# Performance work log

Hardware: AMD Instinct MI355X
Metric: run time of the kernel (lower is better)

## Reference

```python
import jax, jax.numpy as jnp
import numpy as np

B, T, D, HD = 8, 2048, 1024, 64

def setup_inputs() -> dict:
    key = jax.random.key(0)
    k1, k2, k3, k4 = jax.random.split(key, 4)
    x = jax.random.normal(k1, (B, T, D), dtype=jnp.float32)
    Wq = jax.random.normal(k2, (D, HD), dtype=jnp.float32) * (D ** -0.5)
    Wk = jax.random.normal(k3, (D, HD), dtype=jnp.float32) * (D ** -0.5)
    Wv = jax.random.normal(k4, (D, HD), dtype=jnp.float32) * (D ** -0.5)
    return {"x": x, "Wq": Wq, "Wk": Wk, "Wv": Wv}

def reference(x, Wq, Wk, Wv):
    # x: [B,T,D]; projections: [D,HD]
    q = jnp.einsum('btd,dh->bth', x, Wq)
    k = jnp.einsum('btd,dh->bth', x, Wk)
    v = jnp.einsum('btd,dh->bth', x, Wv)
    hd = q.shape[-1]
    scores = jnp.einsum('bth,bsh->bts', q, k) * (hd ** -0.5)  # [B,T,T]
    t = scores.shape[-1]
    causal = jnp.tril(jnp.ones((t, t), dtype=bool))
    scores = jnp.where(causal, scores, -jnp.inf)
    w = jax.nn.softmax(scores, axis=-1)
    # dropout p=0.0 (eval) -> identity
    return jnp.einsum('bts,bsh->bth', w, v)
```

## Files before the change

kernel.cpp:

```cpp
#include <hip/hip_runtime.h>
#include <hip/hip_bf16.h>
#include <stdint.h>

#define NB 8
#define TT 2048
#define DD 1024
#define HDIM 64

typedef __bf16 bf16x8 __attribute__((ext_vector_type(8)));
typedef float f32x4 __attribute__((ext_vector_type(4)));

static_assert(sizeof(bf16x8) == 16, "bf16x8 must be 16 bytes");

__device__ inline ushort f2bf_bits(float f) {
    __hip_bfloat16 h = __float2bfloat16(f);
    return *reinterpret_cast<ushort*>(&h);
}
__device__ inline float bfbits2f(ushort u) {
    unsigned v = ((unsigned)u) << 16;
    return __builtin_bit_cast(float, v);
}
__device__ inline bf16x8 ldb8(const ushort* p) {
    return *reinterpret_cast<const bf16x8*>(p);
}

typedef __attribute__((address_space(3))) uint32_t lds_u32;
typedef const __attribute__((address_space(1))) uint32_t glb_u32;
__device__ inline void gl_lds16(const void* g, void* l) {
    __builtin_amdgcn_global_load_lds((glb_u32*)g, (lds_u32*)l, 16, 0, 0);
}

#define WCNT_VM2   0xF72
#define WCNT_VM3   0xF73
#define WCNT_VM4   0xF74
#define WCNT_LGKM0 0xC07F

__device__ inline int probe_f32(const ushort* x) {
    int lane = threadIdx.x & 63;
    int wild = 0;
    #pragma unroll
    for (int j = 0; j < 4; ++j) {
        ushort u = x[(lane * 4 + j) * 32];
        int e = (u >> 7) & 0xFF;
        wild += (e >= 0xC0);
    }
    unsigned long long m = __ballot(wild > 0);
    return __popcll(m) > 8;
}

__global__ __launch_bounds__(256) void k_wt(const ushort* __restrict__ x,
                                            const void* __restrict__ Wq,
                                            const void* __restrict__ Wk,
                                            const void* __restrict__ Wv,
                                            ushort* __restrict__ Wt) {
    int f32m = probe_f32(x);
    int idx = blockIdx.x * 256 + threadIdx.x;
    int mat = idx >> 16;
    int rem = idx & 65535;
    int d = rem >> 6;
    int h = rem & 63;
    const void* W = (mat == 0) ? Wq : (mat == 1) ? Wk : Wv;
    float v;
    if (f32m) v = ((const float*)W)[rem];
    else      v = bfbits2f(((const ushort*)W)[rem]);
    if (mat == 0) v *= 0.18033688011112042f;
    Wt[(size_t)mat * 65536 + (size_t)h * DD + d] = f2bf_bits(v);
}

template <int F32M>
__device__ inline void proj_body(const void* __restrict__ xv,
                                 const ushort* __restrict__ Wt,
                                 ushort* __restrict__ Qw,
                                 ushort* __restrict__ Kw,
                                 ushort* __restrict__ Vtw,
                                 ushort* Bf, float* Af) {
    int tid  = threadIdx.x;
    int w    = tid >> 6;
    int lane = tid & 63;
    int quad = lane >> 4;
    int col  = lane & 15;
    int mt   = w >> 2;
    int nh   = w & 3;
    int m0   = blockIdx.x * 32;

    ushort* Afb = (ushort*)Af;

    auto stage = [&](int buf, int kkk) {
        #pragma unroll
        for (int j = 0; j < 3; ++j) {
            int f  = w * 3 + j;
            int nt = f >> 1, ks = f & 1;
            gl_lds16(Wt + (size_t)(nt * 16 + col) * DD + kkk + ks * 32 + quad * 8,
                     Bf + ((size_t)buf * 24 + f) * 512);
        }
        if (F32M) {
            int amt = w >> 2, ks = (w >> 1) & 1, hf = w & 1;
            gl_lds16((const float*)xv + (size_t)(m0 + amt * 16 + col) * DD
                         + kkk + ks * 32 + hf * 4 + quad * 8,
                     Af + ((((buf * 2 + amt) * 2 + ks) * 2) + hf) * 256);
        } else if (w < 4) {
            int amt = w >> 1, ks = w & 1;
            gl_lds16((const ushort*)xv + (size_t)(m0 + amt * 16 + col) * DD
                         + kkk + ks * 32 + quad * 8,
                     Afb + (((buf * 2 + amt) * 2) + ks) * 512);
        }
    };

    f32x4 acc[3];
    #pragma unroll
    for (int i = 0; i < 3; ++i) acc[i] = (f32x4){0.f,0.f,0.f,0.f};

    stage(0, 0);
    for (int kk = 0; kk < DD; kk += 64) {
        int p  = (kk >> 6) & 1;
        int kn = (kk + 64 < DD) ? kk + 64 : kk;
        stage(p ^ 1, kn);
        if (F32M) {
            __builtin_amdgcn_s_waitcnt(WCNT_VM4);
        } else {
            if (w < 4) __builtin_amdgcn_s_waitcnt(WCNT_VM4);
            else       __builtin_amdgcn_s_waitcnt(WCNT_VM3);
        }
        __builtin_amdgcn_s_barrier();

        #pragma unroll
        for (int ks = 0; ks < 2; ++ks) {
            bf16x8 a;
            if (F32M) {
                f32x4 alo = *reinterpret_cast<const f32x4*>(Af + ((((p * 2 + mt) * 2 + ks) * 2) + 0) * 256 + lane * 4);
                f32x4 ahi = *reinterpret_cast<const f32x4*>(Af + ((((p * 2 + mt) * 2 + ks) * 2) + 1) * 256 + lane * 4);
                #pragma unroll
                for (int j = 0; j < 4; ++j) { a[j] = (__bf16)alo[j]; a[4+j] = (__bf16)ahi[j]; }
            } else {
                a = ldb8(Afb + (((p * 2 + mt) * 2) + ks) * 512 + lane * 8);
            }
            #pragma unroll
            for (int j = 0; j < 3; ++j) {
                int nt = nh * 3 + j;
                bf16x8 b = ldb8(Bf + ((size_t)p * 24 + nt * 2 + ks) * 512 + lane * 8);
                acc[j] = __builtin_amdgcn_mfma_f32_16x16x32_bf16(a, b, acc[j], 0, 0, 0);
            }
        }
        __builtin_amdgcn_s_waitcnt(WCNT_LGKM0);
        __builtin_amdgcn_s_barrier();
    }

    #pragma unroll
    for (int j = 0; j < 3; ++j) {
        int nt  = nh * 3 + j;
        int mat = nt >> 2;
        int h   = (nt & 3) * 16 + col;
        if (mat == 2) {
            #pragma unroll
            for (int r = 0; r < 4; ++r) {
                int row = m0 + mt * 16 + quad * 4 + r;
                int bb = row >> 11;
                int t  = row & (TT - 1);
                Vtw[(size_t)bb * HDIM * TT + (size_t)h * TT + t] = f2bf_bits(acc[j][r]);
            }
        } else {
            ushort* outp = (mat == 0) ? Qw : Kw;
            #pragma unroll
            for (int r = 0; r < 4; ++r) {
                int row = m0 + mt * 16 + quad * 4 + r;
                outp[(size_t)row * HDIM + h] = f2bf_bits(acc[j][r]);
            }
        }
    }
}

__global__ __launch_bounds__(512) void k_proj(const void* __restrict__ xv,
                                              const ushort* __restrict__ Wt,
                                              ushort* __restrict__ Qw,
                                              ushort* __restrict__ Kw,
                                              ushort* __restrict__ Vtw) {
    __shared__ ushort Bf[2 * 24 * 512];
    __shared__ float  Af[2 * 2 * 2 * 2 * 256];
    if (probe_f32((const ushort*)xv)) proj_body<1>(xv, Wt, Qw, Kw, Vtw, Bf, Af);
    else                              proj_body<0>(xv, Wt, Qw, Kw, Vtw, Bf, Af);
}

__global__ __launch_bounds__(256) void k_attn(const ushort* __restrict__ Qw,
                                              const ushort* __restrict__ Kw,
                                              const ushort* __restrict__ Vtw,
                                              ushort* __restrict__ Po,
                                              float* __restrict__ Pl) {
    int w    = threadIdx.x >> 6;
    int lane = threadIdx.x & 63;
    int quad = lane >> 4;
    int col  = lane & 15;
    int bid  = blockIdx.x;
    int b    = bid & 7;
    int idx  = 79 - (bid >> 3);
    int c, g;
    if (idx < 32)      { c = 0; g = idx; }
    else if (idx < 56) { c = 1; g = idx - 24; }
    else if (idx < 72) { c = 2; g = idx - 40; }
    else               { c = 3; g = idx - 48; }
    int qb = 4 * g + w;
    int m0 = qb * 16;
    int Bq = (qb < 32) ? qb : (qb < 64) ? 2*qb - 32 : (qb < 96) ? 3*qb - 96 : 4*qb - 192;
    int pid = b * 320 + Bq + c;

    const ushort* Qb = Qw + (size_t)b * TT * HDIM;
    const ushort* Kb = Kw + (size_t)b * TT * HDIM;
    const ushort* Vb = Vtw + (size_t)b * HDIM * TT;

    __shared__ ushort KVb[2][8][512];
    __shared__ __hip_bfloat16 Pls[4][16][40];

    auto stageKV = [&](int buf, int s) {
        #pragma unroll
        for (int j = 0; j < 2; ++j) {
            int f = w * 2 + j;
            const ushort* gp;
            if (f < 4) {
                int half = f & 1;
                int ro   = (f >> 1) * 16;
                gp = Kb + (size_t)(s + ro + col) * HDIM + half * 32 + quad * 8;
            } else {
                int vg = f - 4;
                gp = Vb + (size_t)(vg * 16 + col) * TT + s + quad * 8;
            }
            gl_lds16(gp, &KVb[buf][f][0]);
        }
    };

    bf16x8 qf0 = ldb8(Qb + (size_t)(m0 + col) * HDIM + quad * 8);
    bf16x8 qf1 = ldb8(Qb + (size_t)(m0 + col) * HDIM + 32 + quad * 8);

    f32x4 o0 = {0.f,0.f,0.f,0.f};
    f32x4 o1 = {0.f,0.f,0.f,0.f};
    f32x4 o2 = {0.f,0.f,0.f,0.f};
    f32x4 o3 = {0.f,0.f,0.f,0.f};
    float rsum[4] = {0.f, 0.f, 0.f, 0.f};

    const int start = c * 512;
    const int end   = min(start + 512, 64 * g + 64);

    stageKV(0, start);
    for (int s0 = start; s0 < end; s0 += 32) {
        int p  = ((s0 - start) >> 5) & 1;
        int sn = (s0 + 32 < end) ? s0 + 32 : s0;
        stageKV(p ^ 1, sn);
        __builtin_amdgcn_s_waitcnt(WCNT_VM2);
        __builtin_amdgcn_s_barrier();

        if (s0 < m0 + 16) {
            bf16x8 ck0l = ldb8(&KVb[p][0][lane * 8]);
            bf16x8 ck0h = ldb8(&KVb[p][1][lane * 8]);
            bf16x8 ck1l = ldb8(&KVb[p][2][lane * 8]);
            bf16x8 ck1h = ldb8(&KVb[p][3][lane * 8]);

            f32x4 S0 = {0.f,0.f,0.f,0.f};
            f32x4 S1 = {0.f,0.f,0.f,0.f};
            S0 = __builtin_amdgcn_mfma_f32_16x16x32_bf16(qf0, ck0l, S0, 0, 0, 0);
            S0 = __builtin_amdgcn_mfma_f32_16x16x32_bf16(qf1, ck0h, S0, 0, 0, 0);
            S1 = __builtin_amdgcn_mfma_f32_16x16x32_bf16(qf0, ck1l, S1, 0, 0, 0);
            S1 = __builtin_amdgcn_mfma_f32_16x16x32_bf16(qf1, ck1h, S1, 0, 0, 0);

            #pragma unroll
            for (int r = 0; r < 4; ++r) {
                int trow = m0 + quad * 4 + r;
                float aa = (s0 + col      > trow) ? -1e30f : S0[r];
                float dd = (s0 + 16 + col > trow) ? -1e30f : S1[r];
                float p0 = exp2f(aa);
                float p1 = exp2f(dd);
                rsum[r] += p0 + p1;
                Pls[w][quad * 4 + r][col]      = __float2bfloat16(p0);
                Pls[w][quad * 4 + r][16 + col] = __float2bfloat16(p1);
            }
            bf16x8 pf = *reinterpret_cast<const bf16x8*>(&Pls[w][col][quad * 8]);

            bf16x8 cv0 = ldb8(&KVb[p][4][lane * 8]);
            bf16x8 cv1 = ldb8(&KVb[p][5][lane * 8]);
            bf16x8 cv2 = ldb8(&KVb[p][6][lane * 8]);
            bf16x8 cv3 = ldb8(&KVb[p][7][lane * 8]);
            o0 = __builtin_amdgcn_mfma_f32_16x16x32_bf16(pf, cv0, o0, 0, 0, 0);
            o1 = __builtin_amdgcn_mfma_f32_16x16x32_bf16(pf, cv1, o1, 0, 0, 0);
            o2 = __builtin_amdgcn_mfma_f32_16x16x32_bf16(pf, cv2, o2, 0, 0, 0);
            o3 = __builtin_amdgcn_mfma_f32_16x16x32_bf16(pf, cv3, o3, 0, 0, 0);
        }
        __builtin_amdgcn_s_waitcnt(WCNT_LGKM0);
        __builtin_amdgcn_s_barrier();
    }

    #pragma unroll
    for (int off = 1; off < 16; off <<= 1) {
        #pragma unroll
        for (int r = 0; r < 4; ++r)
            rsum[r] += __shfl_xor(rsum[r], off, 64);
    }

    ushort* pb = Po + (size_t)pid * 1024;
    #pragma unroll
    for (int r = 0; r < 4; ++r) {
        int row = quad * 4 + r;
        pb[row * 64 + 0*16 + col] = f2bf_bits(o0[r]);
        pb[row * 64 + 1*16 + col] = f2bf_bits(o1[r]);
        pb[row * 64 + 2*16 + col] = f2bf_bits(o2[r]);
        pb[row * 64 + 3*16 + col] = f2bf_bits(o3[r]);
        if (col == 0) Pl[pid * 16 + row] = rsum[r];
    }
}

__global__ __launch_bounds__(256) void k_merge(const ushort* __restrict__ x,
                                               const ushort* __restrict__ Po,
                                               const float* __restrict__ Pl,
                                               void* __restrict__ outv) {
    int f32m = probe_f32(x);
    int wid  = blockIdx.x * 4 + (threadIdx.x >> 6);
    int lane = threadIdx.x & 63;
    int row  = lane >> 2;
    int g    = lane & 3;
    int b    = wid >> 7;
    int qb   = wid & 127;
    int nch  = (qb >> 5) + 1;
    int Bq   = (qb < 32) ? qb : (qb < 64) ? 2*qb - 32 : (qb < 96) ? 3*qb - 96 : 4*qb - 192;
    int pid0 = b * 320 + Bq;

    float L = 0.f;
    #pragma unroll
    for (int c = 0; c < 4; ++c)
        if (c < nch) L += Pl[(pid0 + c) * 16 + row];
    float inv = 1.0f / L;

    float o[16];
    #pragma unroll
    for (int j = 0; j < 16; ++j) o[j] = 0.f;
    #pragma unroll
    for (int c = 0; c < 4; ++c) {
        if (c < nch) {
            const ushort* p = Po + (size_t)(pid0 + c) * 1024 + row * 64 + g * 16;
            bf16x8 v0 = ldb8(p);
            bf16x8 v1 = ldb8(p + 8);
            #pragma unroll
            for (int j = 0; j < 8; ++j) {
                o[j]     += (float)v0[j];
                o[8 + j] += (float)v1[j];
            }
        }
    }

    size_t obase = ((size_t)b * TT + qb * 16 + row) * HDIM + g * 16;
    if (f32m) {
        float* ob = (float*)outv + obase;
        #pragma unroll
        for (int j = 0; j < 16; ++j) ob[j] = o[j] * inv;
    } else {
        ushort* ob = (ushort*)outv + obase;
        #pragma unroll
        for (int j = 0; j < 16; ++j) ob[j] = f2bf_bits(o[j] * inv);
    }
}

extern "C" void kernel_launch(void* const* d_in, const int* in_sizes, int n_in,
                              void* d_out, int out_size, void* d_ws, size_t ws_size,
                              hipStream_t stream) {
    const ushort* x = (const ushort*)d_in[0];
    ushort* Wt  = (ushort*)d_ws;
    ushort* Qw  = Wt + 3 * HDIM * DD;
    ushort* Kw  = Qw + (size_t)NB * TT * HDIM;
    ushort* Vtw = Kw + (size_t)NB * TT * HDIM;
    ushort* Po  = Vtw + (size_t)NB * TT * HDIM;
    float*  Pl  = (float*)(Po + (size_t)2560 * 1024);

    k_wt   <<<768, 256, 0, stream>>>(x, d_in[1], d_in[2], d_in[3], Wt);
    k_proj <<<512, 512, 0, stream>>>(d_in[0], Wt, Qw, Kw, Vtw);
    k_attn <<<640, 256, 0, stream>>>(Qw, Kw, Vtw, Po, Pl);
    k_merge<<<256, 256, 0, stream>>>(x, Po, Pl, d_out);
}
```

Measured before the change: 155.1 us.

## Triple-buffer projection loads and double M-tile per 1024-thread block

The QKV projection kernel now uses 1024-thread blocks covering 64 rows each, which halves the grid so every Wt tile staged in LDS serves twice as many rows. The LDS staging moves from double to triple buffering with a prefetch distance of two, and the load assignment across the 16 waves and the waitcnt thresholds are redistributed to match. The goal is to hide global load latency better and cut redundant weight traffic. In exchange LDS use per block rises and fewer blocks run concurrently, which may lower occupancy.

```diff
diff --git a/kernel.cpp b/kernel.cpp
--- a/kernel.cpp
+++ b/kernel.cpp
@@ -31,8 +31,8 @@
 }
 
 #define WCNT_VM2   0xF72
-#define WCNT_VM3   0xF73
 #define WCNT_VM4   0xF74
+#define WCNT_VM6   0xF76
 #define WCNT_LGKM0 0xC07F
 
 __device__ inline int probe_f32(const ushort* x) {
@@ -81,28 +81,54 @@
     int col  = lane & 15;
     int mt   = w >> 2;
     int nh   = w & 3;
-    int m0   = blockIdx.x * 32;
-
-    ushort* Afb = (ushort*)Af;
+    int m0   = blockIdx.x * 64;
+
+    const float*  xf  = (const float*)xv;
+    const ushort* xb  = (const ushort*)xv;
+    ushort*       Afb = (ushort*)Af;
 
     auto stage = [&](int buf, int kkk) {
-        #pragma unroll
-        for (int j = 0; j < 3; ++j) {
-            int f  = w * 3 + j;
-            int nt = f >> 1, ks = f & 1;
-            gl_lds16(Wt + (size_t)(nt * 16 + col) * DD + kkk + ks * 32 + quad * 8,
-                     Bf + ((size_t)buf * 24 + f) * 512);
-        }
         if (F32M) {
-            int amt = w >> 2, ks = (w >> 1) & 1, hf = w & 1;
-            gl_lds16((const float*)xv + (size_t)(m0 + amt * 16 + col) * DD
-                         + kkk + ks * 32 + hf * 4 + quad * 8,
-                     Af + ((((buf * 2 + amt) * 2 + ks) * 2) + hf) * 256);
-        } else if (w < 4) {
-            int amt = w >> 1, ks = w & 1;
-            gl_lds16((const ushort*)xv + (size_t)(m0 + amt * 16 + col) * DD
-                         + kkk + ks * 32 + quad * 8,
-                     Afb + (((buf * 2 + amt) * 2) + ks) * 512);
+            if (w < 8) {
+                #pragma unroll
+                for (int j = 0; j < 2; ++j) {
+                    int f  = w * 2 + j;
+                    int nt = f >> 1, ks = f & 1;
+                    gl_lds16(Wt + (size_t)(nt * 16 + col) * DD + kkk + ks * 32 + quad * 8,
+                             Bf + ((size_t)buf * 24 + f) * 512);
+                }
+                int a = w;
+                gl_lds16(xf + (size_t)(m0 + (a >> 2) * 16 + col) * DD
+                             + kkk + ((a >> 1) & 1) * 32 + (a & 1) * 4 + quad * 8,
+                         Af + ((size_t)buf * 16 + a) * 256);
+            } else {
+                int f  = 16 + (w - 8);
+                int nt = f >> 1, ks = f & 1;
+                gl_lds16(Wt + (size_t)(nt * 16 + col) * DD + kkk + ks * 32 + quad * 8,
+                         Bf + ((size_t)buf * 24 + f) * 512);
+                int a = w;
+                gl_lds16(xf + (size_t)(m0 + (a >> 2) * 16 + col) * DD
+                             + kkk + ((a >> 1) & 1) * 32 + (a & 1) * 4 + quad * 8,
+                         Af + ((size_t)buf * 16 + a) * 256);
+            }
+        } else {
+            if (w < 12) {
+                #pragma unroll
+                for (int j = 0; j < 2; ++j) {
+                    int f  = w * 2 + j;
+                    int nt = f >> 1, ks = f & 1;
+                    gl_lds16(Wt + (size_t)(nt * 16 + col) * DD + kkk + ks * 32 + quad * 8,
+                             Bf + ((size_t)buf * 24 + f) * 512);
+                }
+            } else {
+                #pragma unroll
+                for (int j = 0; j < 2; ++j) {
+                    int a = (w - 12) * 2 + j;
+                    gl_lds16(xb + (size_t)(m0 + (a >> 1) * 16 + col) * DD
+                                 + kkk + (a & 1) * 32 + quad * 8,
+                             Afb + ((size_t)buf * 8 + a) * 512);
+                }
+            }
         }
     };
 
@@ -111,15 +137,17 @@
     for (int i = 0; i < 3; ++i) acc[i] = (f32x4){0.f,0.f,0.f,0.f};
 
     stage(0, 0);
+    stage(1, 64);
     for (int kk = 0; kk < DD; kk += 64) {
-        int p  = (kk >> 6) & 1;
-        int kn = (kk + 64 < DD) ? kk + 64 : kk;
-        stage(p ^ 1, kn);
+        int t   = kk >> 6;
+        int p   = t % 3;
+        int kn2 = (kk + 128 < DD) ? kk + 128 : kk;
+        stage((p + 2) % 3, kn2);
         if (F32M) {
+            if (w < 8) __builtin_amdgcn_s_waitcnt(WCNT_VM6);
+            else       __builtin_amdgcn_s_waitcnt(WCNT_VM4);
+        } else {
             __builtin_amdgcn_s_waitcnt(WCNT_VM4);
-        } else {
-            if (w < 4) __builtin_amdgcn_s_waitcnt(WCNT_VM4);
-            else       __builtin_amdgcn_s_waitcnt(WCNT_VM3);
         }
         __builtin_amdgcn_s_barrier();
 
@@ -127,12 +155,12 @@
         for (int ks = 0; ks < 2; ++ks) {
             bf16x8 a;
             if (F32M) {
-                f32x4 alo = *reinterpret_cast<const f32x4*>(Af + ((((p * 2 + mt) * 2 + ks) * 2) + 0) * 256 + lane * 4);
-                f32x4 ahi = *reinterpret_cast<const f32x4*>(Af + ((((p * 2 + mt) * 2 + ks) * 2) + 1) * 256 + lane * 4);
+                f32x4 alo = *reinterpret_cast<const f32x4*>(Af + ((size_t)p * 16 + ((mt * 2 + ks) * 2 + 0)) * 256 + lane * 4);
+                f32x4 ahi = *reinterpret_cast<const f32x4*>(Af + ((size_t)p * 16 + ((mt * 2 + ks) * 2 + 1)) * 256 + lane * 4);
                 #pragma unroll
                 for (int j = 0; j < 4; ++j) { a[j] = (__bf16)alo[j]; a[4+j] = (__bf16)ahi[j]; }
             } else {
-                a = ldb8(Afb + (((p * 2 + mt) * 2) + ks) * 512 + lane * 8);
+                a = ldb8(Afb + ((size_t)p * 8 + mt * 2 + ks) * 512 + lane * 8);
             }
             #pragma unroll
             for (int j = 0; j < 3; ++j) {
@@ -169,13 +197,13 @@
     }
 }
 
-__global__ __launch_bounds__(512) void k_proj(const void* __restrict__ xv,
-                                              const ushort* __restrict__ Wt,
-                                              ushort* __restrict__ Qw,
-                                              ushort* __restrict__ Kw,
-                                              ushort* __restrict__ Vtw) {
-    __shared__ ushort Bf[2 * 24 * 512];
-    __shared__ float  Af[2 * 2 * 2 * 2 * 256];
+__global__ __launch_bounds__(1024) void k_proj(const void* __restrict__ xv,
+                                               const ushort* __restrict__ Wt,
+                                               ushort* __restrict__ Qw,
+                                               ushort* __restrict__ Kw,
+                                               ushort* __restrict__ Vtw) {
+    __shared__ ushort Bf[3 * 24 * 512];
+    __shared__ float  Af[3 * 16 * 256];
     if (probe_f32((const ushort*)xv)) proj_body<1>(xv, Wt, Qw, Kw, Vtw, Bf, Af);
     else                              proj_body<0>(xv, Wt, Qw, Kw, Vtw, Bf, Af);
 }
@@ -366,7 +394,7 @@
     float*  Pl  = (float*)(Po + (size_t)2560 * 1024);
 
     k_wt   <<<768, 256, 0, stream>>>(x, d_in[1], d_in[2], d_in[3], Wt);
-    k_proj <<<512, 512, 0, stream>>>(d_in[0], Wt, Qw, Kw, Vtw);
+    k_proj <<<256, 1024, 0, stream>>>(d_in[0], Wt, Qw, Kw, Vtw);
     k_attn <<<640, 256, 0, stream>>>(Qw, Kw, Vtw, Po, Pl);
     k_merge<<<256, 256, 0, stream>>>(x, Po, Pl, d_out);
 }
```

Measured after the change: 153.3 us. About the same (-1.2%).

## Restructure QKV projection with pre-swizzled weights, register-staged A and triple-buffered B

Applied to the files above, without the earlier changes.

The weight transpose kernel now writes Wt directly in the MFMA fragment layout, so each B tile is staged with contiguous 16-byte global-to-LDS copies. The projection kernel moves to 64-row tiles with 1024 threads per block, which halves the number of blocks and doubles reuse of each staged B tile. x is loaded into registers one step ahead and converted to bf16 once before being written to LDS, replacing the per-MFMA f32-to-bf16 conversion from LDS. B is triple-buffered with a two-step prefetch distance to hide global latency. The cost is more LDS per block, larger blocks that may lower occupancy, and more complex waitcnt accounting.

```diff
diff --git a/kernel.cpp b/kernel.cpp
--- a/kernel.cpp
+++ b/kernel.cpp
@@ -9,6 +9,7 @@
 
 typedef __bf16 bf16x8 __attribute__((ext_vector_type(8)));
 typedef float f32x4 __attribute__((ext_vector_type(4)));
+typedef ushort u16x4 __attribute__((ext_vector_type(4)));
 
 static_assert(sizeof(bf16x8) == 16, "bf16x8 must be 16 bytes");
 
@@ -32,7 +33,7 @@
 
 #define WCNT_VM2   0xF72
 #define WCNT_VM3   0xF73
-#define WCNT_VM4   0xF74
+#define WCNT_VM5   0xF75
 #define WCNT_LGKM0 0xC07F
 
 __device__ inline int probe_f32(const ushort* x) {
@@ -64,7 +65,11 @@
     if (f32m) v = ((const float*)W)[rem];
     else      v = bfbits2f(((const ushort*)W)[rem]);
     if (mat == 0) v *= 0.18033688011112042f;
-    Wt[(size_t)mat * 65536 + (size_t)h * DD + d] = f2bf_bits(v);
+    int n    = mat * 64 + h;
+    int nt   = n >> 4, ncol = n & 15;
+    int kk   = d >> 6, ks = (d >> 5) & 1, qd = (d >> 3) & 3, e = d & 7;
+    int f    = nt * 2 + ks;
+    Wt[((size_t)(kk * 24 + f)) * 512 + (qd * 16 + ncol) * 8 + e] = f2bf_bits(v);
 }
 
 template <int F32M>
@@ -73,7 +78,7 @@
                                  ushort* __restrict__ Qw,
                                  ushort* __restrict__ Kw,
                                  ushort* __restrict__ Vtw,
-                                 ushort* Bf, float* Af) {
+                                 ushort* Bf, ushort* Afb) {
     int tid  = threadIdx.x;
     int w    = tid >> 6;
     int lane = tid & 63;
@@ -81,59 +86,74 @@
     int col  = lane & 15;
     int mt   = w >> 2;
     int nh   = w & 3;
-    int m0   = blockIdx.x * 32;
-
-    ushort* Afb = (ushort*)Af;
-
-    auto stage = [&](int buf, int kkk) {
-        #pragma unroll
-        for (int j = 0; j < 3; ++j) {
-            int f  = w * 3 + j;
-            int nt = f >> 1, ks = f & 1;
-            gl_lds16(Wt + (size_t)(nt * 16 + col) * DD + kkk + ks * 32 + quad * 8,
+    int m0   = blockIdx.x * 64;
+
+    const float*  xf = (const float*)xv;
+    const ushort* xb = (const ushort*)xv;
+
+    auto stageB = [&](int buf, int kkk) {
+        int kk24 = (kkk >> 6) * 24;
+        if (w < 8) {
+            #pragma unroll
+            for (int j = 0; j < 2; ++j) {
+                int f = w * 2 + j;
+                gl_lds16(Wt + ((size_t)(kk24 + f)) * 512 + lane * 8,
+                         Bf + ((size_t)buf * 24 + f) * 512);
+            }
+        } else {
+            int f = 16 + (w - 8);
+            gl_lds16(Wt + ((size_t)(kk24 + f)) * 512 + lane * 8,
                      Bf + ((size_t)buf * 24 + f) * 512);
         }
+    };
+
+    int arow = m0 + w * 4 + quad;
+    int aa   = (w >> 2) * 2 + (col >> 3);
+    int aoff = (((col & 7) >> 1) * 16 + (w & 3) * 4 + quad) * 8
+             + (col & 1) * 4;
+
+    f32x4 ar_f;
+    u16x4 ar_b;
+    auto loadA = [&](int kkk) {
+        if (F32M) ar_f = *reinterpret_cast<const f32x4*>(xf + (size_t)arow * DD + kkk + col * 4);
+        else      ar_b = *reinterpret_cast<const u16x4*>(xb + (size_t)arow * DD + kkk + col * 4);
+    };
+    auto writeA = [&](int q) {
+        u16x4 v;
         if (F32M) {
-            int amt = w >> 2, ks = (w >> 1) & 1, hf = w & 1;
-            gl_lds16((const float*)xv + (size_t)(m0 + amt * 16 + col) * DD
-                         + kkk + ks * 32 + hf * 4 + quad * 8,
-                     Af + ((((buf * 2 + amt) * 2 + ks) * 2) + hf) * 256);
-        } else if (w < 4) {
-            int amt = w >> 1, ks = w & 1;
-            gl_lds16((const ushort*)xv + (size_t)(m0 + amt * 16 + col) * DD
-                         + kkk + ks * 32 + quad * 8,
-                     Afb + (((buf * 2 + amt) * 2) + ks) * 512);
-        }
+            #pragma unroll
+            for (int j = 0; j < 4; ++j) v[j] = f2bf_bits(ar_f[j]);
+        } else {
+            v = ar_b;
+        }
+        *reinterpret_cast<u16x4*>(Afb + ((size_t)q * 8 + aa) * 512 + aoff) = v;
     };
 
     f32x4 acc[3];
     #pragma unroll
     for (int i = 0; i < 3; ++i) acc[i] = (f32x4){0.f,0.f,0.f,0.f};
 
-    stage(0, 0);
-    for (int kk = 0; kk < DD; kk += 64) {
-        int p  = (kk >> 6) & 1;
-        int kn = (kk + 64 < DD) ? kk + 64 : kk;
-        stage(p ^ 1, kn);
-        if (F32M) {
-            __builtin_amdgcn_s_waitcnt(WCNT_VM4);
-        } else {
-            if (w < 4) __builtin_amdgcn_s_waitcnt(WCNT_VM4);
-            else       __builtin_amdgcn_s_waitcnt(WCNT_VM3);
-        }
+    loadA(0);
+    stageB(0, 0);
+    stageB(1, 64);
+    writeA(0);
+    __builtin_amdgcn_s_waitcnt(WCNT_LGKM0);
+
+    for (int t = 0; t < 16; ++t) {
+        int p   = t % 3;
+        int p2  = (t + 2) % 3;
+        int kn1 = (t + 1 < 16) ? (t + 1) * 64 : 960;
+        int kn2 = (t + 2 < 16) ? (t + 2) * 64 : 960;
+        loadA(kn1);
+        stageB(p2, kn2);
+        if (w < 8) __builtin_amdgcn_s_waitcnt(WCNT_VM5);
+        else       __builtin_amdgcn_s_waitcnt(WCNT_VM3);
         __builtin_amdgcn_s_barrier();
 
+        int q = t & 1;
         #pragma unroll
         for (int ks = 0; ks < 2; ++ks) {
-            bf16x8 a;
-            if (F32M) {
-                f32x4 alo = *reinterpret_cast<const f32x4*>(Af + ((((p * 2 + mt) * 2 + ks) * 2) + 0) * 256 + lane * 4);
-                f32x4 ahi = *reinterpret_cast<const f32x4*>(Af + ((((p * 2 + mt) * 2 + ks) * 2) + 1) * 256 + lane * 4);
-                #pragma unroll
-                for (int j = 0; j < 4; ++j) { a[j] = (__bf16)alo[j]; a[4+j] = (__bf16)ahi[j]; }
-            } else {
-                a = ldb8(Afb + (((p * 2 + mt) * 2) + ks) * 512 + lane * 8);
-            }
+            bf16x8 a = ldb8(Afb + ((size_t)q * 8 + mt * 2 + ks) * 512 + lane * 8);
             #pragma unroll
             for (int j = 0; j < 3; ++j) {
                 int nt = nh * 3 + j;
@@ -141,6 +161,7 @@
                 acc[j] = __builtin_amdgcn_mfma_f32_16x16x32_bf16(a, b, acc[j], 0, 0, 0);
             }
         }
+        writeA(q ^ 1);
         __builtin_amdgcn_s_waitcnt(WCNT_LGKM0);
         __builtin_amdgcn_s_barrier();
     }
@@ -169,15 +190,15 @@
     }
 }
 
-__global__ __launch_bounds__(512) void k_proj(const void* __restrict__ xv,
-                                              const ushort* __restrict__ Wt,
-                                              ushort* __restrict__ Qw,
-                                              ushort* __restrict__ Kw,
-                                              ushort* __restrict__ Vtw) {
-    __shared__ ushort Bf[2 * 24 * 512];
-    __shared__ float  Af[2 * 2 * 2 * 2 * 256];
-    if (probe_f32((const ushort*)xv)) proj_body<1>(xv, Wt, Qw, Kw, Vtw, Bf, Af);
-    else                              proj_body<0>(xv, Wt, Qw, Kw, Vtw, Bf, Af);
+__global__ __launch_bounds__(1024) void k_proj(const void* __restrict__ xv,
+                                               const ushort* __restrict__ Wt,
+                                               ushort* __restrict__ Qw,
+                                               ushort* __restrict__ Kw,
+                                               ushort* __restrict__ Vtw) {
+    __shared__ ushort Bf[3 * 24 * 512];
+    __shared__ ushort Afb[2 * 8 * 512];
+    if (probe_f32((const ushort*)xv)) proj_body<1>(xv, Wt, Qw, Kw, Vtw, Bf, Afb);
+    else                              proj_body<0>(xv, Wt, Qw, Kw, Vtw, Bf, Afb);
 }
 
 __global__ __launch_bounds__(256) void k_attn(const ushort* __restrict__ Qw,
@@ -366,7 +387,7 @@
     float*  Pl  = (float*)(Po + (size_t)2560 * 1024);
 
     k_wt   <<<768, 256, 0, stream>>>(x, d_in[1], d_in[2], d_in[3], Wt);
-    k_proj <<<512, 512, 0, stream>>>(d_in[0], Wt, Qw, Kw, Vtw);
+    k_proj <<<256, 1024, 0, stream>>>(d_in[0], Wt, Qw, Kw, Vtw);
     k_attn <<<640, 256, 0, stream>>>(Qw, Kw, Vtw, Po, Pl);
     k_merge<<<256, 256, 0, stream>>>(x, Po, Pl, d_out);
 }
```

Result: faster. 144.6 us (-6.8%).
